# Performance work log

Measured on AMD Instinct MI355X. Metric: run time of the kernel, lower is better.

The kernel has to match this reference:

```python
import jax, jax.numpy as jnp
import numpy as np

WORLD_SIZE = 1
EXPERT_NUM = 8
D_MODEL = 1024
D_HIDDEN = 4096
TOK_PER_EXPERT = 2048


def setup_inputs() -> dict:
    key = jax.random.key(0)
    k1, k2, k3 = jax.random.split(key, 3)
    x = jax.random.normal(k1, (EXPERT_NUM, TOK_PER_EXPERT, D_MODEL), dtype=jnp.float32)
    # kaiming_uniform-like scale for faithfulness of magnitudes
    bound1 = 1.0 / np.sqrt(D_MODEL)
    bound2 = 1.0 / np.sqrt(D_HIDDEN)
    weight1 = jax.random.uniform(k2, (EXPERT_NUM, D_HIDDEN, D_MODEL), dtype=jnp.float32, minval=-bound1, maxval=bound1)
    weight2 = jax.random.uniform(k3, (EXPERT_NUM, D_MODEL, D_HIDDEN), dtype=jnp.float32, minval=-bound2, maxval=bound2)
    return {"x": x, "weight1": weight1, "weight2": weight2}


def reference(x, weight1, weight2):
    # x -> (world_size, expert_num, tokens, d_model)
    xr = x.reshape(WORLD_SIZE, EXPERT_NUM, -1, D_MODEL)
    # grouped GEMM 1 + ReLU: [g,e,s,m] x [e,h,m] -> [g,e,s,h]
    ffn1 = jax.nn.relu(jnp.einsum('gesm,ehm->gesh', xr, weight1))
    # grouped GEMM 2: [g,e,s,h] x [e,m,h] -> [g,e,s,m]
    y = jnp.einsum('gesh,emh->gesm', ffn1, weight2)
    return y
```

## Files before the change

### kernel.cpp

```cpp
#include <hip/hip_runtime.h>
#include <hip/hip_bf16.h>

#define EXPERTS 8
#define TOK 2048
#define DM 1024
#define DH 4096

#define BM 128
#define BN 128
#define BK 32
#define LSTR 40

typedef __bf16 bf16x8 __attribute__((ext_vector_type(8)));
typedef float  f32x4  __attribute__((ext_vector_type(4)));

static __device__ __forceinline__ bf16x8 cvt8(float4 a, float4 b) {
    bf16x8 r;
    r[0] = (__bf16)a.x; r[1] = (__bf16)a.y; r[2] = (__bf16)a.z; r[3] = (__bf16)a.w;
    r[4] = (__bf16)b.x; r[5] = (__bf16)b.y; r[6] = (__bf16)b.z; r[7] = (__bf16)b.w;
    return r;
}

static __device__ __forceinline__ void gload16(const __bf16* g, __bf16* l) {
    __builtin_amdgcn_global_load_lds(
        (__attribute__((address_space(1))) void*)g,
        (__attribute__((address_space(3))) void*)l, 16, 0, 0);
}

#define BARRIER() asm volatile("s_barrier" ::: "memory")
#define SB()      __builtin_amdgcn_sched_barrier(0)
#define LGKM0()   do { asm volatile("s_waitcnt lgkmcnt(0)" ::: "memory"); SB(); } while (0)
#define VMW0()    do { asm volatile("s_waitcnt vmcnt(0)" ::: "memory"); SB(); } while (0)

__global__ __launch_bounds__(256)
void cvt_all(const float* __restrict__ x,  const float* __restrict__ w1,
             const float* __restrict__ w2, __bf16* __restrict__ xb,
             __bf16* __restrict__ w1b,     __bf16* __restrict__ w2b,
             int nx, int nw1, int ntot) {
    int i = blockIdx.x * blockDim.x + threadIdx.x;
    const int stride = gridDim.x * blockDim.x;
    for (; i < ntot; i += stride) {
        const float* src; __bf16* dst; int off;
        if (i < nx)            { src = x;  dst = xb;  off = i; }
        else if (i < nx + nw1) { src = w1; dst = w1b; off = i - nx; }
        else                   { src = w2; dst = w2b; off = i - nx - nw1; }
        const float4* p = (const float4*)src + (size_t)off * 2;
        float4 a = p[0], b = p[1];
        *((bf16x8*)dst + off) = cvt8(a, b);
    }
}

template<bool RELU, bool OUT_BF16>
__global__ __launch_bounds__(512, 4)
void gemm_sb(const __bf16* __restrict__ Ap, const __bf16* __restrict__ Bp,
             void* __restrict__ Cp, int N, int K, int tiles_m, int tiles_n,
             size_t sA, size_t sB, size_t sC)
{
    __shared__ __bf16 lds[16384 + 8192];

    int bid = blockIdx.x;
    const int chunk = gridDim.x >> 3;
    bid = (bid & 7) * chunk + (bid >> 3);

    const int per_e = tiles_m * tiles_n;
    const int e  = bid / per_e;
    const int tt = bid - e * per_e;
    const int tn = tt / tiles_m;
    const int tm = tt - tn * tiles_m;

    const int tid = threadIdx.x;
    const int l   = tid & 63;
    const int wid = tid >> 6;
    const int wr  = wid >> 1;
    const int wc  = wid & 1;
    const int lr  = l & 15;
    const int kg  = l >> 4;
    const int lq  = l >> 3;
    const int swz_e = ((l & 7) ^ lq) << 3;

    const int cc0  = (kg * 16) ^ ((l & 7) << 4);
    const int cc1  = cc0 ^ 64;
    const int rowA = (wr * 64 + lr) * 128;
    const int rowB = (wc * 64 + lr) * 128;

    const __bf16* Ag = Ap + e * sA + (size_t)(tm * 256) * K;
    const __bf16* Bg = Bp + e * sB + (size_t)(tn * 128) * K;

    auto stage_u = [&](const __bf16* g, int base_e, int u, int kt2) {
        const __bf16* s0 = g + (size_t)(u * 64 + wid * 8 + lq) * K + kt2 * 64 + swz_e;
        gload16(s0, &lds[base_e + u * 4096 + wid * 512]);
    };

    f32x4 acc[4][4];
    #pragma unroll
    for (int m = 0; m < 4; ++m)
        #pragma unroll
        for (int n = 0; n < 4; ++n)
            acc[m][n] = (f32x4){0.f, 0.f, 0.f, 0.f};

    const char* Ab = (const char*)&lds[0] + rowA;
    const char* Bb = (const char*)&lds[16384] + rowB;

    bf16x8 a[4], b[4];

    const int NT = K / 64;

    #pragma unroll
    for (int u = 0; u < 4; ++u) stage_u(Ag, 0, u, 0);
    #pragma unroll
    for (int u = 0; u < 2; ++u) stage_u(Bg, 16384, u, 0);

    for (int t = 0; t < NT; ++t) {
        const bool pf = (t + 1 < NT);

        VMW0();
        BARRIER();

        #pragma unroll
        for (int mf = 0; mf < 4; ++mf) a[mf] = *(const bf16x8*)(Ab + mf * 2048 + cc0);
        #pragma unroll
        for (int nf = 0; nf < 4; ++nf) b[nf] = *(const bf16x8*)(Bb + nf * 2048 + cc0);
        LGKM0();
        #pragma unroll
        for (int mf = 0; mf < 4; ++mf)
            #pragma unroll
            for (int nf = 0; nf < 4; ++nf)
                acc[mf][nf] = __builtin_amdgcn_mfma_f32_16x16x32_bf16(
                    a[mf], b[nf], acc[mf][nf], 0, 0, 0);
        SB();

        #pragma unroll
        for (int mf = 0; mf < 4; ++mf) a[mf] = *(const bf16x8*)(Ab + mf * 2048 + cc1);
        #pragma unroll
        for (int nf = 0; nf < 4; ++nf) b[nf] = *(const bf16x8*)(Bb + nf * 2048 + cc1);
        LGKM0();
        BARRIER();

        if (pf) {
            #pragma unroll
            for (int u = 0; u < 4; ++u) stage_u(Ag, 0, u, t + 1);
            #pragma unroll
            for (int u = 0; u < 2; ++u) stage_u(Bg, 16384, u, t + 1);
        }
        #pragma unroll
        for (int mf = 0; mf < 4; ++mf)
            #pragma unroll
            for (int nf = 0; nf < 4; ++nf)
                acc[mf][nf] = __builtin_amdgcn_mfma_f32_16x16x32_bf16(
                    a[mf], b[nf], acc[mf][nf], 0, 0, 0);
    }

    const int orow = tm * 256 + wr * 64 + kg * 4;
    const int ocol = tn * 128 + wc * 64 + lr;
    if constexpr (OUT_BF16) {
        __bf16* C = (__bf16*)Cp + e * sC;
        #pragma unroll
        for (int mf = 0; mf < 4; ++mf)
            #pragma unroll
            for (int j = 0; j < 4; ++j) {
                const size_t base = (size_t)(orow + mf * 16 + j) * N + ocol;
                #pragma unroll
                for (int nf = 0; nf < 4; ++nf) {
                    float v = acc[mf][nf][j];
                    if (RELU) v = fmaxf(v, 0.f);
                    C[base + nf * 16] = (__bf16)v;
                }
            }
    } else {
        float* C = (float*)Cp + e * sC;
        #pragma unroll
        for (int mf = 0; mf < 4; ++mf)
            #pragma unroll
            for (int j = 0; j < 4; ++j) {
                const size_t base = (size_t)(orow + mf * 16 + j) * N + ocol;
                #pragma unroll
                for (int nf = 0; nf < 4; ++nf) {
                    float v = acc[mf][nf][j];
                    if (RELU) v = fmaxf(v, 0.f);
                    C[base + nf * 16] = v;
                }
            }
    }
}

template<int AMODE, int BMODE, bool RELU, bool OUT_BF16>
__global__ __launch_bounds__(256)
void gemm2(const void* __restrict__ Ap, const void* __restrict__ Bp,
           void* __restrict__ Cp, int N, int K, int tiles_m, int tiles_n,
           size_t sA, size_t sB, size_t sC)
{
    constexpr int LA = (AMODE == 0) ? BK : LSTR;
    constexpr int LB = (BMODE == 0) ? BK : LSTR;
    __shared__ __bf16 As[BM * LA];
    __shared__ __bf16 Bs[BN * LB];

    int bid = blockIdx.x;
    const int chunk = gridDim.x >> 3;
    bid = (bid & 7) * chunk + (bid >> 3);

    const int per_e = tiles_m * tiles_n;
    const int e  = bid / per_e;
    const int t  = bid - e * per_e;
    const int tn = t / tiles_m;
    const int tm = t - tn * tiles_m;

    const int tid = threadIdx.x;
    const int l   = tid & 63;
    const int wid = tid >> 6;
    const int wr  = wid >> 1, wc = wid & 1;
    const int lr  = l & 15;
    const int kg  = l >> 4;
    const int srow = tid >> 1;
    const int scol = (tid & 1) << 4;

    const __bf16* gA = nullptr; __bf16* lA = nullptr;
    const float*  pAf = nullptr; __bf16* aWr = nullptr;
    float4 A0, A1, A2, A3;
    if constexpr (AMODE == 0) {
        gA = (const __bf16*)Ap + e * sA
           + (size_t)(tm * BM + wid * 16 + (l >> 2)) * K + (l & 3) * 8;
        lA = As + wid * 512;
    } else {
        pAf = (const float*)Ap + e * sA + (size_t)(tm * BM + srow) * K + scol;
        aWr = As + srow * LA + scol;
        A0 = *(const float4*)(pAf);      A1 = *(const float4*)(pAf + 4);
        A2 = *(const float4*)(pAf + 8);  A3 = *(const float4*)(pAf + 12);
    }
    const __bf16* gB = nullptr; __bf16* lB = nullptr;
    const float*  pBf = nullptr; __bf16* bWr = nullptr;
    float4 B0, B1, B2, B3;
    if constexpr (BMODE == 0) {
        gB = (const __bf16*)Bp + e * sB
           + (size_t)(tn * BN + wid * 16 + (l >> 2)) * K + (l & 3) * 8;
        lB = Bs + wid * 512;
    } else {
        pBf = (const float*)Bp + e * sB + (size_t)(tn * BN + srow) * K + scol;
        bWr = Bs + srow * LB + scol;
        B0 = *(const float4*)(pBf);      B1 = *(const float4*)(pBf + 4);
        B2 = *(const float4*)(pBf + 8);  B3 = *(const float4*)(pBf + 12);
    }

    const __bf16* aRd = As + (wr * 64 + lr) * LA + kg * 8;
    const __bf16* bRd = Bs + (wc * 64 + lr) * LB + kg * 8;

    f32x4 acc[4][4];
    #pragma unroll
    for (int m = 0; m < 4; ++m)
        #pragma unroll
        for (int n = 0; n < 4; ++n)
            acc[m][n] = (f32x4){0.f, 0.f, 0.f, 0.f};

    const int NT = K / BK;
    for (int kt = 0; kt < NT; ++kt) {
        if (kt) __syncthreads();
        if constexpr (AMODE == 0) {
            gload16(gA, lA);
            gload16(gA + (size_t)64 * K, lA + 2048);
            gA += BK;
        } else {
            *(bf16x8*)(aWr)     = cvt8(A0, A1);
            *(bf16x8*)(aWr + 8) = cvt8(A2, A3);
        }
        if constexpr (BMODE == 0) {
            gload16(gB, lB);
            gload16(gB + (size_t)64 * K, lB + 2048);
            gB += BK;
        } else {
            *(bf16x8*)(bWr)     = cvt8(B0, B1);
            *(bf16x8*)(bWr + 8) = cvt8(B2, B3);
        }
        __syncthreads();

        if (kt + 1 < NT) {
            if constexpr (AMODE == 2) {
                pAf += BK;
                A0 = *(const float4*)(pAf);      A1 = *(const float4*)(pAf + 4);
                A2 = *(const float4*)(pAf + 8);  A3 = *(const float4*)(pAf + 12);
            }
            if constexpr (BMODE == 2) {
                pBf += BK;
                B0 = *(const float4*)(pBf);      B1 = *(const float4*)(pBf + 4);
                B2 = *(const float4*)(pBf + 8);  B3 = *(const float4*)(pBf + 12);
            }
        }

        bf16x8 af[4], bfr[4];
        #pragma unroll
        for (int m = 0; m < 4; ++m) af[m]  = *(const bf16x8*)(aRd + m * 16 * LA);
        #pragma unroll
        for (int n = 0; n < 4; ++n) bfr[n] = *(const bf16x8*)(bRd + n * 16 * LB);
        #pragma unroll
        for (int m = 0; m < 4; ++m)
            #pragma unroll
            for (int n = 0; n < 4; ++n)
                acc[m][n] = __builtin_amdgcn_mfma_f32_16x16x32_bf16(af[m], bfr[n], acc[m][n], 0, 0, 0);
    }

    const int orow = tm * BM + wr * 64 + kg * 4;
    const int ocol = tn * BN + wc * 64 + lr;
    if constexpr (OUT_BF16) {
        __bf16* C = (__bf16*)Cp + e * sC;
        #pragma unroll
        for (int m = 0; m < 4; ++m)
            #pragma unroll
            for (int j = 0; j < 4; ++j) {
                const size_t base = (size_t)(orow + m * 16 + j) * N + ocol;
                #pragma unroll
                for (int n = 0; n < 4; ++n) {
                    float v = acc[m][n][j];
                    if (RELU) v = fmaxf(v, 0.f);
                    C[base + n * 16] = (__bf16)v;
                }
            }
    } else {
        float* C = (float*)Cp + e * sC;
        #pragma unroll
        for (int m = 0; m < 4; ++m)
            #pragma unroll
            for (int j = 0; j < 4; ++j) {
                const size_t base = (size_t)(orow + m * 16 + j) * N + ocol;
                #pragma unroll
                for (int n = 0; n < 4; ++n) {
                    float v = acc[m][n][j];
                    if (RELU) v = fmaxf(v, 0.f);
                    C[base + n * 16] = v;
                }
            }
    }
}

extern "C" void kernel_launch(void* const* d_in, const int* in_sizes, int n_in,
                              void* d_out, int out_size, void* d_ws, size_t ws_size,
                              hipStream_t stream) {
    const float* x  = (const float*)d_in[0];
    const float* w1 = (const float*)d_in[1];
    const float* w2 = (const float*)d_in[2];
    float* out = (float*)d_out;

    const size_t SZ_F  = (size_t)EXPERTS * TOK * DH * sizeof(__bf16);
    const size_t SZ_X  = (size_t)EXPERTS * TOK * DM * sizeof(__bf16);
    const size_t SZ_W1 = (size_t)EXPERTS * DH * DM * sizeof(__bf16);
    const size_t SZ_W2 = (size_t)EXPERTS * DM * DH * sizeof(__bf16);

    char* wsb = (char*)d_ws;
    __bf16* ffn1 = (__bf16*)wsb;

    const dim3 blk(256);
    const dim3 cgrid(2048);
    const int NX  = EXPERTS * TOK * DM / 8;
    const int NW1 = EXPERTS * DH * DM / 8;
    const int NW2 = EXPERTS * DM * DH / 8;

    const size_t eA1 = (size_t)TOK * DM, eB1 = (size_t)DH * DM, eC1 = (size_t)TOK * DH;
    const size_t eA2 = (size_t)TOK * DH, eB2 = (size_t)DM * DH, eC2 = (size_t)TOK * DM;

    if (ws_size >= SZ_F + SZ_X + SZ_W1 + SZ_W2) {
        __bf16* xb  = (__bf16*)(wsb + SZ_F);
        __bf16* w1b = (__bf16*)(wsb + SZ_F + SZ_X);
        __bf16* w2b = (__bf16*)(wsb + SZ_F + SZ_X + SZ_W1);
        hipLaunchKernelGGL(cvt_all, cgrid, blk, 0, stream,
            x, w1, w2, xb, w1b, w2b, NX, NW1, NX + NW1 + NW2);
        const dim3 g1(EXPERTS * (TOK / 256) * (DH / 128));
        const dim3 g2(EXPERTS * (TOK / 256) * (DM / 128));
        hipLaunchKernelGGL((gemm_sb<true, true>), g1, dim3(512), 0, stream,
            xb, w1b, ffn1, DH, DM, TOK / 256, DH / 128, eA1, eB1, eC1);
        hipLaunchKernelGGL((gemm_sb<false, false>), g2, dim3(512), 0, stream,
            ffn1, w2b, out, DM, DH, TOK / 256, DM / 128, eA2, eB2, eC2);
    } else if (ws_size >= SZ_F + SZ_X + SZ_W1) {
        __bf16* xb  = (__bf16*)(wsb + SZ_F);
        __bf16* w1b = (__bf16*)(wsb + SZ_F + SZ_X);
        hipLaunchKernelGGL(cvt_all, cgrid, blk, 0, stream,
            x, w1, w1, xb, w1b, w1b, NX, NW1, NX + NW1);
        const dim3 g1(EXPERTS * (TOK / 256) * (DH / 128));
        const dim3 g2(EXPERTS * (TOK / BM) * (DM / BN));
        hipLaunchKernelGGL((gemm_sb<true, true>), g1, dim3(512), 0, stream,
            xb, w1b, ffn1, DH, DM, TOK / 256, DH / 128, eA1, eB1, eC1);
        hipLaunchKernelGGL((gemm2<0, 2, false, false>), g2, blk, 0, stream,
            ffn1, w2, out, DM, DH, TOK / BM, DM / BN, eA2, eB2, eC2);
    } else if (ws_size >= SZ_F + SZ_W1) {
        __bf16* w1b = (__bf16*)(wsb + SZ_F);
        hipLaunchKernelGGL(cvt_all, cgrid, blk, 0, stream,
            w1, w1, w1, w1b, w1b, w1b, NW1, 0, NW1);
        const dim3 g1(EXPERTS * (TOK / BM) * (DH / BN));
        const dim3 g2(EXPERTS * (TOK / BM) * (DM / BN));
        hipLaunchKernelGGL((gemm2<2, 0, true, true>), g1, blk, 0, stream,
            x, w1b, ffn1, DH, DM, TOK / BM, DH / BN, eA1, eB1, eC1);
        hipLaunchKernelGGL((gemm2<0, 2, false, false>), g2, blk, 0, stream,
            ffn1, w2, out, DM, DH, TOK / BM, DM / BN, eA2, eB2, eC2);
    } else if (ws_size >= SZ_F) {
        const dim3 g1(EXPERTS * (TOK / BM) * (DH / BN));
        const dim3 g2(EXPERTS * (TOK / BM) * (DM / BN));
        hipLaunchKernelGGL((gemm2<2, 2, true, true>), g1, blk, 0, stream,
            x, w1, ffn1, DH, DM, TOK / BM, DH / BN, eA1, eB1, eC1);
        hipLaunchKernelGGL((gemm2<0, 2, false, false>), g2, blk, 0, stream,
            ffn1, w2, out, DM, DH, TOK / BM, DM / BN, eA2, eB2, eC2);
    } else {
        int rows = (int)((ws_size / ((size_t)DH * sizeof(__bf16))) / BM) * BM;
        if (rows <= 0) rows = BM;
        if (rows > TOK) rows = TOK;
        for (int e = 0; e < EXPERTS; ++e) {
            for (int r0 = 0; r0 < TOK; r0 += rows) {
                int mr = (TOK - r0 < rows) ? (TOK - r0) : rows;
                dim3 cg1((mr / BM) * (DH / BN));
                hipLaunchKernelGGL((gemm2<2, 2, true, true>), cg1, blk, 0, stream,
                    x + ((size_t)e * TOK + r0) * DM, w1 + (size_t)e * DH * DM, ffn1,
                    DH, DM, mr / BM, DH / BN, (size_t)0, (size_t)0, (size_t)0);
                dim3 cg2((mr / BM) * (DM / BN));
                hipLaunchKernelGGL((gemm2<0, 2, false, false>), cg2, blk, 0, stream,
                    ffn1, w2 + (size_t)e * DM * DH, out + ((size_t)e * TOK + r0) * DM,
                    DM, DH, mr / BM, DM / BN, (size_t)0, (size_t)0, (size_t)0);
            }
        }
    }
}
```

Measured before the change: 365.1 us.

## Replace 8-wave single-buffer GEMM with 4-wave double-buffered interleaved pipeline

Swaps the 512-thread, 256x128-tile GEMM with a single LDS buffer for a 256-thread, 128x128-tile kernel that double-buffers LDS and splits each K step into fine-grained chunks. Global-to-LDS loads for the next tiles are interleaved between MFMA groups, guarded by partial vmcnt/lgkmcnt waits. The aim is to hide global load latency and LDS reads behind matrix math rather than stalling on a full vmcnt(0) at every step. In exchange it adds more barriers, doubles the grid size, and depends on fragile hand-written waitcnt ordering.

```diff
diff --git a/kernel.cpp b/kernel.cpp
--- a/kernel.cpp
+++ b/kernel.cpp
@@ -30,7 +30,9 @@
 #define BARRIER() asm volatile("s_barrier" ::: "memory")
 #define SB()      __builtin_amdgcn_sched_barrier(0)
 #define LGKM0()   do { asm volatile("s_waitcnt lgkmcnt(0)" ::: "memory"); SB(); } while (0)
-#define VMW0()    do { asm volatile("s_waitcnt vmcnt(0)" ::: "memory"); SB(); } while (0)
+#define LGKM2()   do { asm volatile("s_waitcnt lgkmcnt(2)" ::: "memory"); SB(); } while (0)
+#define VMW4()    asm volatile("s_waitcnt vmcnt(4)" ::: "memory")
+#define VMW0()    asm volatile("s_waitcnt vmcnt(0)" ::: "memory")
 
 __global__ __launch_bounds__(256)
 void cvt_all(const float* __restrict__ x,  const float* __restrict__ w1,
@@ -51,12 +53,12 @@
 }
 
 template<bool RELU, bool OUT_BF16>
-__global__ __launch_bounds__(512, 4)
-void gemm_sb(const __bf16* __restrict__ Ap, const __bf16* __restrict__ Bp,
-             void* __restrict__ Cp, int N, int K, int tiles_m, int tiles_n,
-             size_t sA, size_t sB, size_t sC)
+__global__ __launch_bounds__(256, 2)
+void gemm4w(const __bf16* __restrict__ Ap, const __bf16* __restrict__ Bp,
+            void* __restrict__ Cp, int N, int K, int tiles_m, int tiles_n,
+            size_t sA, size_t sB, size_t sC)
 {
-    __shared__ __bf16 lds[16384 + 8192];
+    __shared__ __bf16 lds[2][2][8192];
 
     int bid = blockIdx.x;
     const int chunk = gridDim.x >> 3;
@@ -83,12 +85,13 @@
     const int rowA = (wr * 64 + lr) * 128;
     const int rowB = (wc * 64 + lr) * 128;
 
-    const __bf16* Ag = Ap + e * sA + (size_t)(tm * 256) * K;
+    const __bf16* Ag = Ap + e * sA + (size_t)(tm * 128) * K;
     const __bf16* Bg = Bp + e * sB + (size_t)(tn * 128) * K;
 
-    auto stage_u = [&](const __bf16* g, int base_e, int u, int kt2) {
+    auto stage_u = [&](const __bf16* g, int mat, int c2, int u, int kt2) {
         const __bf16* s0 = g + (size_t)(u * 64 + wid * 8 + lq) * K + kt2 * 64 + swz_e;
-        gload16(s0, &lds[base_e + u * 4096 + wid * 512]);
+        gload16(s0,                  &lds[c2][mat][u * 4096 + wid * 512]);
+        gload16(s0 + (size_t)32 * K, &lds[c2][mat][u * 4096 + 2048 + wid * 512]);
     };
 
     f32x4 acc[4][4];
@@ -98,59 +101,109 @@
         for (int n = 0; n < 4; ++n)
             acc[m][n] = (f32x4){0.f, 0.f, 0.f, 0.f};
 
-    const char* Ab = (const char*)&lds[0] + rowA;
-    const char* Bb = (const char*)&lds[16384] + rowB;
-
-    bf16x8 a[4], b[4];
+    const char* A0b = (const char*)&lds[0][0][0] + rowA;
+    const char* B0b = (const char*)&lds[0][1][0] + rowB;
+    const char* A1b = (const char*)&lds[1][0][0] + rowA;
+    const char* B1b = (const char*)&lds[1][1][0] + rowB;
+
+    bf16x8 a[4][2], blo[2][2], bhi[2][2];
+
+    auto rdA_k = [&](const char* base, int kk) {
+        const int cc = kk ? cc1 : cc0;
+        #pragma unroll
+        for (int mf = 0; mf < 4; ++mf)
+            a[mf][kk] = *(const bf16x8*)(base + mf * 2048 + cc);
+    };
+    auto rdB_k = [&](bf16x8 (&dst)[2][2], const char* base, int half, int kk) {
+        const int cc = kk ? cc1 : cc0;
+        #pragma unroll
+        for (int nf = 0; nf < 2; ++nf)
+            dst[nf][kk] = *(const bf16x8*)(base + (half * 2 + nf) * 2048 + cc);
+    };
+    auto mma8 = [&](bf16x8 (&b2)[2][2], int no, int kk) {
+        #pragma unroll
+        for (int mf = 0; mf < 4; ++mf)
+            #pragma unroll
+            for (int nf = 0; nf < 2; ++nf)
+                acc[mf][no + nf] = __builtin_amdgcn_mfma_f32_16x16x32_bf16(
+                    a[mf][kk], b2[nf][kk], acc[mf][no + nf], 0, 0, 0);
+    };
 
     const int NT = K / 64;
-
-    #pragma unroll
-    for (int u = 0; u < 4; ++u) stage_u(Ag, 0, u, 0);
-    #pragma unroll
-    for (int u = 0; u < 2; ++u) stage_u(Bg, 16384, u, 0);
-
-    for (int t = 0; t < NT; ++t) {
-        const bool pf = (t + 1 < NT);
-
-        VMW0();
-        BARRIER();
-
-        #pragma unroll
-        for (int mf = 0; mf < 4; ++mf) a[mf] = *(const bf16x8*)(Ab + mf * 2048 + cc0);
-        #pragma unroll
-        for (int nf = 0; nf < 4; ++nf) b[nf] = *(const bf16x8*)(Bb + nf * 2048 + cc0);
-        LGKM0();
-        #pragma unroll
-        for (int mf = 0; mf < 4; ++mf)
-            #pragma unroll
-            for (int nf = 0; nf < 4; ++nf)
-                acc[mf][nf] = __builtin_amdgcn_mfma_f32_16x16x32_bf16(
-                    a[mf], b[nf], acc[mf][nf], 0, 0, 0);
+    const int NI = NT / 2;
+
+    stage_u(Ag, 0, 0, 0, 0); stage_u(Ag, 0, 0, 1, 0);
+    stage_u(Bg, 1, 0, 0, 0); stage_u(Bg, 1, 0, 1, 0);
+    stage_u(Bg, 1, 1, 0, 1); stage_u(Bg, 1, 1, 1, 1);
+
+    for (int it = 0; it < NI; ++it) {
+        const int To = 2 * it + 1;
+        const int Te = 2 * it + 2;
+        const int Tn = 2 * it + 3;
+        const bool pf = (it + 1 < NI);
+
+        VMW4();
+        BARRIER();
+        rdB_k(blo, B0b, 0, 0);
+        rdA_k(A0b, 0);
         SB();
-
-        #pragma unroll
-        for (int mf = 0; mf < 4; ++mf) a[mf] = *(const bf16x8*)(Ab + mf * 2048 + cc1);
-        #pragma unroll
-        for (int nf = 0; nf < 4; ++nf) b[nf] = *(const bf16x8*)(Bb + nf * 2048 + cc1);
-        LGKM0();
-        BARRIER();
-
-        if (pf) {
-            #pragma unroll
-            for (int u = 0; u < 4; ++u) stage_u(Ag, 0, u, t + 1);
-            #pragma unroll
-            for (int u = 0; u < 2; ++u) stage_u(Bg, 16384, u, t + 1);
-        }
-        #pragma unroll
-        for (int mf = 0; mf < 4; ++mf)
-            #pragma unroll
-            for (int nf = 0; nf < 4; ++nf)
-                acc[mf][nf] = __builtin_amdgcn_mfma_f32_16x16x32_bf16(
-                    a[mf], b[nf], acc[mf][nf], 0, 0, 0);
-    }
-
-    const int orow = tm * 256 + wr * 64 + kg * 4;
+        rdB_k(blo, B0b, 0, 1);
+        stage_u(Ag, 0, 1, 0, To);
+        LGKM2();
+        mma8(blo, 0, 0);
+        LGKM0();
+
+        rdB_k(bhi, B0b, 1, 0);
+        SB();
+        rdB_k(bhi, B0b, 1, 1);
+        BARRIER();
+        stage_u(Ag, 0, 1, 1, To);
+        LGKM2();
+        mma8(bhi, 2, 0);
+        LGKM0();
+
+        rdA_k(A0b, 1);
+        BARRIER();
+        if (pf) stage_u(Bg, 1, 0, 0, Te);
+        LGKM0();
+        mma8(bhi, 2, 1);
+
+        BARRIER();
+        if (pf) stage_u(Bg, 1, 0, 1, Te);
+        mma8(blo, 0, 1);
+
+        if (pf) VMW4(); else VMW0();
+        BARRIER();
+        rdB_k(blo, B1b, 0, 0);
+        rdA_k(A1b, 0);
+        SB();
+        rdB_k(blo, B1b, 0, 1);
+        if (pf) stage_u(Ag, 0, 0, 0, Te);
+        LGKM2();
+        mma8(blo, 0, 0);
+        LGKM0();
+
+        rdB_k(bhi, B1b, 1, 0);
+        SB();
+        rdB_k(bhi, B1b, 1, 1);
+        BARRIER();
+        if (pf) stage_u(Ag, 0, 0, 1, Te);
+        LGKM2();
+        mma8(bhi, 2, 0);
+        LGKM0();
+
+        rdA_k(A1b, 1);
+        BARRIER();
+        if (pf) stage_u(Bg, 1, 1, 0, Tn);
+        LGKM0();
+        mma8(bhi, 2, 1);
+
+        BARRIER();
+        if (pf) stage_u(Bg, 1, 1, 1, Tn);
+        mma8(blo, 0, 1);
+    }
+
+    const int orow = tm * 128 + wr * 64 + kg * 4;
     const int ocol = tn * 128 + wc * 64 + lr;
     if constexpr (OUT_BF16) {
         __bf16* C = (__bf16*)Cp + e * sC;
@@ -360,21 +413,21 @@
         __bf16* w2b = (__bf16*)(wsb + SZ_F + SZ_X + SZ_W1);
         hipLaunchKernelGGL(cvt_all, cgrid, blk, 0, stream,
             x, w1, w2, xb, w1b, w2b, NX, NW1, NX + NW1 + NW2);
-        const dim3 g1(EXPERTS * (TOK / 256) * (DH / 128));
-        const dim3 g2(EXPERTS * (TOK / 256) * (DM / 128));
-        hipLaunchKernelGGL((gemm_sb<true, true>), g1, dim3(512), 0, stream,
-            xb, w1b, ffn1, DH, DM, TOK / 256, DH / 128, eA1, eB1, eC1);
-        hipLaunchKernelGGL((gemm_sb<false, false>), g2, dim3(512), 0, stream,
-            ffn1, w2b, out, DM, DH, TOK / 256, DM / 128, eA2, eB2, eC2);
+        const dim3 g1(EXPERTS * (TOK / 128) * (DH / 128));
+        const dim3 g2(EXPERTS * (TOK / 128) * (DM / 128));
+        hipLaunchKernelGGL((gemm4w<true, true>), g1, blk, 0, stream,
+            xb, w1b, ffn1, DH, DM, TOK / 128, DH / 128, eA1, eB1, eC1);
+        hipLaunchKernelGGL((gemm4w<false, false>), g2, blk, 0, stream,
+            ffn1, w2b, out, DM, DH, TOK / 128, DM / 128, eA2, eB2, eC2);
     } else if (ws_size >= SZ_F + SZ_X + SZ_W1) {
         __bf16* xb  = (__bf16*)(wsb + SZ_F);
         __bf16* w1b = (__bf16*)(wsb + SZ_F + SZ_X);
         hipLaunchKernelGGL(cvt_all, cgrid, blk, 0, stream,
             x, w1, w1, xb, w1b, w1b, NX, NW1, NX + NW1);
-        const dim3 g1(EXPERTS * (TOK / 256) * (DH / 128));
+        const dim3 g1(EXPERTS * (TOK / 128) * (DH / 128));
         const dim3 g2(EXPERTS * (TOK / BM) * (DM / BN));
-        hipLaunchKernelGGL((gemm_sb<true, true>), g1, dim3(512), 0, stream,
-            xb, w1b, ffn1, DH, DM, TOK / 256, DH / 128, eA1, eB1, eC1);
+        hipLaunchKernelGGL((gemm4w<true, true>), g1, blk, 0, stream,
+            xb, w1b, ffn1, DH, DM, TOK / 128, DH / 128, eA1, eB1, eC1);
         hipLaunchKernelGGL((gemm2<0, 2, false, false>), g2, blk, 0, stream,
             ffn1, w2, out, DM, DH, TOK / BM, DM / BN, eA2, eB2, eC2);
     } else if (ws_size >= SZ_F + SZ_W1) {
```

After: 387.7 us. +6.2%, slower.
